# Kernel optimization log

Hardware: AMD Instinct MI355X
Metric: run time of the kernel (lower is better)

## Reference

```python
import jax, jax.numpy as jnp
import numpy as np

NH, HS, K = 32, 2048, 16
HD = HS // NH
B, L = 4, 2048
EPS = 1e-6

def _ln(x, gamma, beta):
    mu = x.mean(-1, keepdims=True)
    var = x.var(-1, keepdims=True)  # ddof=0 == torch unbiased=False
    return gamma * ((x - mu) / jnp.sqrt(var + EPS)) + beta

def _ln_fused_l2_bwd(x, target, gamma, beta):
    D = x.shape[-1]
    mu = x.mean(-1, keepdims=True)
    std = jnp.sqrt(x.var(-1, keepdims=True) + EPS)
    xh = (x - mu) / std
    gxh = (gamma * xh + beta - target) * gamma
    return (D * gxh - gxh.sum(-1, keepdims=True) - xh * (gxh * xh).sum(-1, keepdims=True)) / (D * std)

def setup_inputs() -> dict:
    key = jax.random.key(0)
    ks = jax.random.split(key, 8)
    s = 0.02
    return {
        'hidden_states': jax.random.normal(ks[0], (B, L, HS), jnp.float32),
        'position_ids': jnp.tile(jnp.arange(L, dtype=jnp.int32)[None], (B, 1)),
        'q_w': jax.random.normal(ks[1], (HS, HS), jnp.float32) * s,
        'k_w': jax.random.normal(ks[2], (HS, HS), jnp.float32) * s,
        'v_w': jax.random.normal(ks[3], (HS, HS), jnp.float32) * s,
        'o_w': jax.random.normal(ks[4], (HS, HS), jnp.float32) * s,
        'W1': jax.random.normal(ks[5], (NH, HD, HD), jnp.float32) * s,
        'b1': jnp.zeros((NH, 1, HD), jnp.float32),
        'ttt_norm_weight': jnp.ones((NH, HD), jnp.float32),
        'ttt_norm_bias': jnp.zeros((NH, HD), jnp.float32),
        'ttt_lr_weight': jax.random.normal(ks[6], (NH, 1, HS), jnp.float32) * s,
        'ttt_lr_bias': jnp.zeros((NH, 1), jnp.float32),
        'learnable_token_idx': jnp.zeros((K,), jnp.float32),
        'post_norm_weight': jnp.ones((HS,), jnp.float32),
        'post_norm_bias': jnp.zeros((HS,), jnp.float32),
    }

def _forward(hidden_states, q_w, k_w, v_w, o_w, W1, b1, ttt_norm_weight,
             ttt_norm_bias, ttt_lr_weight, ttt_lr_bias, learnable_token_idx,
             post_norm_weight, post_norm_bias):
    Bb, Ll, _ = hidden_states.shape
    NM = Ll // K

    def proj_heads(w):
        return (hidden_states @ w.T).reshape(Bb, Ll, NH, HD).transpose(0, 2, 1, 3)

    XQ = proj_heads(q_w).reshape(Bb, NH, NM, K, HD)
    XK = proj_heads(k_w).reshape(Bb, NH, NM, K, HD)
    XV = proj_heads(v_w).reshape(Bb, NH, NM, K, HD)
    X = hidden_states.reshape(Bb, NM, K, HS)

    # eta: learned per-token lr gate, [B,nh,NM,K,K]
    ttt_lr = jnp.einsum('bnkc,hdc->bhnkd', X, ttt_lr_weight) + ttt_lr_bias.reshape(1, NH, 1, 1, 1)
    ttt_lr_eta = jax.nn.sigmoid(ttt_lr).transpose(0, 1, 2, 4, 3) / HD  # ttt_base_lr = 1.0
    token_idx = jnp.clip(1.0 / jnp.arange(1, K + 1, dtype=jnp.float32) + learnable_token_idx, 0.0, None)
    eta = token_idx.reshape(1, 1, 1, K, 1) * ttt_lr_eta

    ln_w = ttt_norm_weight.reshape(NH, 1, HD)
    ln_b = ttt_norm_bias.reshape(NH, 1, HD)

    def step(carry, x):
        W1_s, b1_s = carry                 # [B,nh,hd,hd], [B,nh,1,hd]
        xq, xk, xv, eta_mb = x             # [B,nh,K,hd], eta_mb [B,nh,K,K]
        Z1 = xk @ W1_s + b1_s
        grad = _ln_fused_l2_bwd(Z1, xv - xk, ln_w, ln_b)
        Attn1 = jnp.tril(xq @ xk.swapaxes(-1, -2))
        b1_bar = b1_s - jnp.tril(eta_mb) @ grad
        Z1_bar = xq @ W1_s - (eta_mb * Attn1) @ grad + b1_bar
        last_eta = eta_mb[:, :, -1, :, None]  # [B,nh,K,1]
        W1_new = W1_s - (last_eta * xk).swapaxes(-1, -2) @ grad
        b1_new = b1_s - jnp.sum(last_eta * grad, axis=-2, keepdims=True)
        out = xq + _ln(Z1_bar, ln_w, ln_b)
        return (W1_new, b1_new), out

    init = (jnp.tile(W1[None], (Bb, 1, 1, 1)), jnp.tile(b1[None], (Bb, 1, 1, 1)))
    xs = (XQ.transpose(2, 0, 1, 3, 4), XK.transpose(2, 0, 1, 3, 4),
          XV.transpose(2, 0, 1, 3, 4), eta.transpose(2, 0, 1, 3, 4))
    _, ys = jax.lax.scan(step, init, xs)          # [NM,B,nh,K,hd]
    out = ys.transpose(1, 0, 3, 2, 4).reshape(Bb, Ll, HS)
    out = _ln(out, post_norm_weight, post_norm_bias)  # post_norm (eps 1e-6)
    return out @ o_w.T

def reference(hidden_states, position_ids, q_w, k_w, v_w, o_w, W1, b1,
              ttt_norm_weight, ttt_norm_bias, ttt_lr_weight, ttt_lr_bias,
              learnable_token_idx, post_norm_weight, post_norm_bias):
    del position_ids  # unused in the shown forward (rope never applied)
    return _forward(hidden_states, q_w, k_w, v_w, o_w, W1, b1, ttt_norm_weight,
                    ttt_norm_bias, ttt_lr_weight, ttt_lr_bias, learnable_token_idx,
                    post_norm_weight, post_norm_bias)
```

## Files before the change

### kernel.cpp

```cpp
#include <hip/hip_runtime.h>

typedef unsigned short u16;
typedef unsigned int u32;
typedef __bf16 bf16_t;
typedef bf16_t bf16x4 __attribute__((ext_vector_type(4)));
typedef bf16_t bf16x8 __attribute__((ext_vector_type(8)));
typedef float f32x4 __attribute__((ext_vector_type(4)));
typedef u16 u16x4 __attribute__((ext_vector_type(4)));
typedef u16 u16x8 __attribute__((ext_vector_type(8)));
typedef short s16x4 __attribute__((ext_vector_type(4)));

#define B_   4
#define L_   2048
#define HS_  2048
#define NH_  32
#define HD_  64
#define KK_  16
#define NM_  128
#define M_   (B_*L_)

__device__ __forceinline__ u16 f2bf(float f) {
  unsigned u = __float_as_uint(f);
  u += 0x7FFFu + ((u >> 16) & 1u);
  return (u16)(u >> 16);
}
__device__ __forceinline__ float bf2f(u16 u) {
  return __uint_as_float(((unsigned)u) << 16);
}
__device__ __forceinline__ s16x4 pk4(float a, float b, float c, float d) {
  bf16x4 v;
  v[0] = (__bf16)a; v[1] = (__bf16)b; v[2] = (__bf16)c; v[3] = (__bf16)d;
  return __builtin_bit_cast(s16x4, v);
}

__device__ __forceinline__ f32x4 mfma16(s16x4 a, s16x4 b, f32x4 c) {
  return __builtin_amdgcn_mfma_f32_16x16x16bf16_1k(a, b, c, 0, 0, 0);
}

template <int CTRL>
__device__ __forceinline__ float dpp_add(float v) {
  int t = __builtin_amdgcn_update_dpp(0, __builtin_bit_cast(int, v), CTRL, 0xF, 0xF, true);
  return v + __builtin_bit_cast(float, t);
}
template <int CTRL>
__device__ __forceinline__ f32x4 dpp_add4(f32x4 v) {
  f32x4 r;
#pragma unroll
  for (int i = 0; i < 4; ++i) r[i] = dpp_add<CTRL>(v[i]);
  return r;
}
__device__ __forceinline__ f32x4 row_reduce16(f32x4 v) {
  v = dpp_add4<0x121>(v);
  v = dpp_add4<0x122>(v);
  v = dpp_add4<0x124>(v);
  v = dpp_add4<0x128>(v);
  return v;
}

__global__ __launch_bounds__(256) void cast_f32_bf16(const float* __restrict__ in,
                                                     u16* __restrict__ out, int n) {
  int i = (blockIdx.x * 256 + threadIdx.x) * 8;
  if (i >= n) return;
  float4 a = *(const float4*)(in + i);
  float4 b = *(const float4*)(in + i + 4);
  u16x8 o;
  o[0]=f2bf(a.x); o[1]=f2bf(a.y); o[2]=f2bf(a.z); o[3]=f2bf(a.w);
  o[4]=f2bf(b.x); o[5]=f2bf(b.y); o[6]=f2bf(b.z); o[7]=f2bf(b.w);
  *(u16x8*)(out + i) = o;
}

#define BM 128
#define BN 128
#define BK 32
#define LDT 40

template <bool BF16OUT>
__global__ __launch_bounds__(256) void gemm_nt(const u16* __restrict__ A,
                                               const u16* __restrict__ Bt,
                                               void* __restrict__ Cv,
                                               int M, int N, int K) {
  __shared__ u16 As[BM * LDT];
  __shared__ u16 Bs[BN * LDT];
  int tid  = threadIdx.x;
  int lane = tid & 63, wave = tid >> 6;
  int quad = lane >> 4, l16 = lane & 15;
  int bM = blockIdx.x * BM, bN = blockIdx.y * BN;
  int wM = (wave >> 1) * 64, wN = (wave & 1) * 64;
  int r0 = tid >> 2, c0 = (tid & 3) * 8;
  const u16* Ap = A + (size_t)bM * K;
  const u16* Bp = Bt + (size_t)bN * K;
  f32x4 acc[4][4] = {};
  u16x8 pa0 = *(const u16x8*)(Ap + (size_t)r0 * K + c0);
  u16x8 pa1 = *(const u16x8*)(Ap + (size_t)(r0 + 64) * K + c0);
  u16x8 pb0 = *(const u16x8*)(Bp + (size_t)r0 * K + c0);
  u16x8 pb1 = *(const u16x8*)(Bp + (size_t)(r0 + 64) * K + c0);
  int nk = K / BK;
  for (int kt = 0; kt < nk; ++kt) {
    *(u16x8*)&As[r0 * LDT + c0]        = pa0;
    *(u16x8*)&As[(r0 + 64) * LDT + c0] = pa1;
    *(u16x8*)&Bs[r0 * LDT + c0]        = pb0;
    *(u16x8*)&Bs[(r0 + 64) * LDT + c0] = pb1;
    __syncthreads();
    if (kt + 1 < nk) {
      int k0 = (kt + 1) * BK + c0;
      pa0 = *(const u16x8*)(Ap + (size_t)r0 * K + k0);
      pa1 = *(const u16x8*)(Ap + (size_t)(r0 + 64) * K + k0);
      pb0 = *(const u16x8*)(Bp + (size_t)r0 * K + k0);
      pb1 = *(const u16x8*)(Bp + (size_t)(r0 + 64) * K + k0);
    }
    bf16x8 af[4], bfr[4];
#pragma unroll
    for (int i = 0; i < 4; ++i) {
      u16x8 t = *(const u16x8*)&As[(wM + i * 16 + l16) * LDT + quad * 8];
      af[i] = __builtin_bit_cast(bf16x8, t);
    }
#pragma unroll
    for (int j = 0; j < 4; ++j) {
      u16x8 t = *(const u16x8*)&Bs[(wN + j * 16 + l16) * LDT + quad * 8];
      bfr[j] = __builtin_bit_cast(bf16x8, t);
    }
#pragma unroll
    for (int i = 0; i < 4; ++i) {
#pragma unroll
      for (int j = 0; j < 4; ++j)
        acc[i][j] = __builtin_amdgcn_mfma_f32_16x16x32_bf16(af[i], bfr[j], acc[i][j], 0, 0, 0);
    }
    __syncthreads();
  }
#pragma unroll
  for (int i = 0; i < 4; ++i) {
#pragma unroll
    for (int j = 0; j < 4; ++j) {
      int row = bM + wM + i * 16 + quad * 4;
      int col = bN + wN + j * 16 + l16;
      if (BF16OUT) {
        u16* cp = (u16*)Cv + (size_t)row * N + col;
#pragma unroll
        for (int r = 0; r < 4; ++r) cp[(size_t)r * N] = f2bf(acc[i][j][r]);
      } else {
        float* cp = (float*)Cv + (size_t)row * N + col;
#pragma unroll
        for (int r = 0; r < 4; ++r) cp[(size_t)r * N] = acc[i][j][r];
      }
    }
  }
}

__global__ __launch_bounds__(256) void sig_kernel(const u16* __restrict__ hsb,
                                                  const u16* __restrict__ lrwb,
                                                  const float* __restrict__ lrb,
                                                  float* __restrict__ Sig) {
  __shared__ u16 Bs[32 * LDT];
  int tid = threadIdx.x;
  int lane = tid & 63, wave = tid >> 6;
  int quad = lane >> 4, l16 = lane & 15;
  int m0 = blockIdx.x * 64 + wave * 16;
  f32x4 acc0 = {}, acc1 = {};
  for (int kt = 0; kt < HS_ / BK; ++kt) {
    int k0 = kt * BK;
    if (tid < 128) {
      int r = tid >> 2, c8 = (tid & 3) * 8;
      *(u16x8*)&Bs[r * LDT + c8] = *(const u16x8*)(lrwb + (size_t)r * HS_ + k0 + c8);
    }
    __syncthreads();
    u16x8 ta = *(const u16x8*)(hsb + (size_t)(m0 + l16) * HS_ + k0 + quad * 8);
    u16x8 t0 = *(const u16x8*)&Bs[l16 * LDT + quad * 8];
    u16x8 t1 = *(const u16x8*)&Bs[(16 + l16) * LDT + quad * 8];
    bf16x8 af  = __builtin_bit_cast(bf16x8, ta);
    bf16x8 bf0 = __builtin_bit_cast(bf16x8, t0);
    bf16x8 bf1 = __builtin_bit_cast(bf16x8, t1);
    acc0 = __builtin_amdgcn_mfma_f32_16x16x32_bf16(af, bf0, acc0, 0, 0, 0);
    acc1 = __builtin_amdgcn_mfma_f32_16x16x32_bf16(af, bf1, acc1, 0, 0, 0);
    __syncthreads();
  }
#pragma unroll
  for (int j = 0; j < 2; ++j) {
    f32x4 a = j ? acc1 : acc0;
    int h = j * 16 + l16;
    float bias = lrb[h];
#pragma unroll
    for (int r = 0; r < 4; ++r) {
      int m = m0 + quad * 4 + r;
      float v = a[r] + bias;
      float s = (1.f / (1.f + expf(-v))) * (1.f / 64.f);
      Sig[(size_t)m * NH_ + h] = s;
    }
  }
}

__global__ __launch_bounds__(64, 1) void ttt_scan_wave(
    const u16* __restrict__ XQ, const u16* __restrict__ XK, const u16* __restrict__ XV,
    const float* __restrict__ Sig, const float* __restrict__ W1_0, const float* __restrict__ b1_0,
    const float* __restrict__ lnw, const float* __restrict__ lnb, const float* __restrict__ lti,
    float* __restrict__ Y) {
  int lane = threadIdx.x;
  int quad = lane >> 4, l16 = lane & 15;
  int bh = blockIdx.x, b = bh >> 5, h = bh & 31;

  s16x4 idB;
#pragma unroll
  for (int jj = 0; jj < 4; ++jj)
    idB[jj] = (l16 == quad * 4 + jj) ? (short)0x3F80 : (short)0;

  f32x4 m2[4][4];
  {
    const float* wsrc = W1_0 + (size_t)h * 4096;
#pragma unroll
    for (int c = 0; c < 4; ++c)
#pragma unroll
      for (int a = 0; a < 4; ++a)
#pragma unroll
        for (int r = 0; r < 4; ++r)
          m2[c][a][r] = wsrc[(size_t)(c * 16 + quad * 4 + r) * 64 + a * 16 + l16];
  }

  f32x4 b1r, gam, bet;
#pragma unroll
  for (int a = 0; a < 4; ++a) {
    b1r[a] = b1_0[h * 64 + a * 16 + l16];
    gam[a] = lnw[h * 64 + a * 16 + l16];
    bet[a] = lnb[h * 64 + a * 16 + l16];
  }
  float tokL  = fmaxf(1.0f / (float)(l16 + 1) + lti[l16], 0.0f);
  float tok15 = fmaxf(1.0f / 16.0f + lti[15], 0.0f);

  size_t gb = ((size_t)(b * L_ + l16)) * HS_ + h * HD_ + quad * 4;
  const float* sigp = Sig + (size_t)(b * L_ + quad * 4) * NH_ + h;

  u16x4 cxk[4], cxq[4], cxv[4];
  f32x4 csig;
#pragma unroll
  for (int c = 0; c < 4; ++c) {
    cxk[c] = *(const u16x4*)(XK + gb + c * 16);
    cxq[c] = *(const u16x4*)(XQ + gb + c * 16);
    cxv[c] = *(const u16x4*)(XV + gb + c * 16);
  }
#pragma unroll
  for (int r = 0; r < 4; ++r) csig[r] = sigp[(size_t)r * NH_];

  for (int n = 0; n < NM_; ++n) {
    s16x4 fwB[4][4];
#pragma unroll
    for (int c = 0; c < 4; ++c)
#pragma unroll
      for (int a = 0; a < 4; ++a)
        fwB[c][a] = pk4(m2[c][a][0], m2[c][a][1], m2[c][a][2], m2[c][a][3]);

    s16x4 fdiff[4];
#pragma unroll
    for (int c = 0; c < 4; ++c) {
      float dv[4];
#pragma unroll
      for (int j = 0; j < 4; ++j) dv[j] = bf2f(cxv[c][j]) - bf2f(cxk[c][j]);
      fdiff[c] = pk4(dv[0], dv[1], dv[2], dv[3]);
    }

    s16x4 fxk[4], fxq[4];
#pragma unroll
    for (int c = 0; c < 4; ++c) {
      fxk[c] = __builtin_bit_cast(s16x4, cxk[c]);
      fxq[c] = __builtin_bit_cast(s16x4, cxq[c]);
    }
    f32x4 sigc = csig;

    if (n + 1 < NM_) {
      size_t g = gb + (size_t)(n + 1) * KK_ * HS_;
#pragma unroll
      for (int c = 0; c < 4; ++c) {
        cxk[c] = *(const u16x4*)(XK + g + c * 16);
        cxq[c] = *(const u16x4*)(XQ + g + c * 16);
        cxv[c] = *(const u16x4*)(XV + g + c * 16);
      }
#pragma unroll
      for (int r = 0; r < 4; ++r)
        csig[r] = sigp[(size_t)((n + 1) * KK_ + r) * NH_];
    }

    f32x4 z1[4] = {}, zq4[4] = {}, atT = {};
    f32x4 ddC[4], xkC[4];
#pragma unroll
    for (int c = 0; c < 4; ++c) {
      f32x4 zz = {};
      atT    = mfma16(fxk[c], fxq[c], atT);
      xkC[c] = mfma16(fxk[c], idB, zz);
      ddC[c] = mfma16(fdiff[c], idB, zz);
#pragma unroll
      for (int a = 0; a < 4; ++a) {
        z1[a]  = mfma16(fxk[c], fwB[c][a], z1[a]);
        zq4[a] = mfma16(fxq[c], fwB[c][a], zq4[a]);
      }
    }

    s16x4 fX[4];
#pragma unroll
    for (int c = 0; c < 4; ++c)
      fX[c] = pk4(-tok15 * xkC[c][0], -tok15 * xkC[c][1],
                  -tok15 * xkC[c][2], -tok15 * xkC[c][3]);

    float cf[4];
#pragma unroll
    for (int r = 0; r < 4; ++r)
      cf[r] = (quad * 4 + r <= l16) ? -tokL * (1.0f + atT[r]) : 0.0f;
    s16x4 fA = pk4(cf[0], cf[1], cf[2], cf[3]);

#pragma unroll
    for (int a = 0; a < 4; ++a)
#pragma unroll
      for (int r = 0; r < 4; ++r) z1[a][r] += b1r[a];
    f32x4 s1 = z1[0] + z1[1] + z1[2] + z1[3];
    f32x4 s2 = z1[0] * z1[0] + z1[1] * z1[1] + z1[2] * z1[2] + z1[3] * z1[3];
    s1 = row_reduce16(s1);
    s2 = row_reduce16(s2);
    f32x4 mu, rstd;
#pragma unroll
    for (int r = 0; r < 4; ++r) {
      mu[r] = s1[r] * (1.0f / 64.0f);
      float var = s2[r] * (1.0f / 64.0f) - mu[r] * mu[r];
      rstd[r] = 1.0f / sqrtf(var + 1e-6f);
    }

    f32x4 xh[4], gxh[4], t1v = {}, t2v = {};
#pragma unroll
    for (int a = 0; a < 4; ++a) {
#pragma unroll
      for (int r = 0; r < 4; ++r) {
        xh[a][r]  = (z1[a][r] - mu[r]) * rstd[r];
        gxh[a][r] = (gam[a] * xh[a][r] + bet[a] - ddC[a][r]) * gam[a];
      }
      t1v = t1v + gxh[a];
      t2v = t2v + gxh[a] * xh[a];
    }
    t1v = row_reduce16(t1v);
    t2v = row_reduce16(t2v);

    s16x4 fG[4];
    float bs[4];
#pragma unroll
    for (int a = 0; a < 4; ++a) {
      float sg[4];
#pragma unroll
      for (int r = 0; r < 4; ++r) {
        float g = (64.0f * gxh[a][r] - t1v[r] - xh[a][r] * t2v[r]) * (rstd[r] * (1.0f / 64.0f));
        sg[r] = sigc[r] * g;
      }
      fG[a] = pk4(sg[0], sg[1], sg[2], sg[3]);
      bs[a] = sg[0] + sg[1] + sg[2] + sg[3];
    }
#pragma unroll
    for (int a = 0; a < 4; ++a) {
      bs[a] += __shfl_xor(bs[a], 16, 64);
      bs[a] += __shfl_xor(bs[a], 32, 64);
    }

    f32x4 zb[4];
#pragma unroll
    for (int a = 0; a < 4; ++a) {
      zb[a] = mfma16(fA, fG[a], zq4[a]);
#pragma unroll
      for (int r = 0; r < 4; ++r) zb[a][r] += b1r[a];
    }
#pragma unroll
    for (int a = 0; a < 4; ++a) b1r[a] -= tok15 * bs[a];

#pragma unroll
    for (int c = 0; c < 4; ++c)
#pragma unroll
      for (int a = 0; a < 4; ++a)
        m2[c][a] = mfma16(fX[c], fG[a], m2[c][a]);

    f32x4 w1s = zb[0] + zb[1] + zb[2] + zb[3];
    f32x4 w2s = zb[0] * zb[0] + zb[1] * zb[1] + zb[2] * zb[2] + zb[3] * zb[3];
    w1s = row_reduce16(w1s);
    w2s = row_reduce16(w2s);
#pragma unroll
    for (int r = 0; r < 4; ++r) {
      float mu2 = w1s[r] * (1.0f / 64.0f);
      float var2 = w2s[r] * (1.0f / 64.0f) - mu2 * mu2;
      float rstd2 = 1.0f / sqrtf(var2 + 1e-6f);
      float* yp = Y + ((size_t)(b * L_ + n * KK_ + quad * 4 + r)) * HS_ + h * HD_ + l16;
#pragma unroll
      for (int a = 0; a < 4; ++a)
        yp[a * 16] = gam[a] * ((zb[a][r] - mu2) * rstd2) + bet[a];
    }
  }
}

__global__ __launch_bounds__(256) void postnorm(const float* __restrict__ Yin,
                                                const u16* __restrict__ XQr,
                                                const float* __restrict__ w,
                                                const float* __restrict__ bb,
                                                u16* __restrict__ Yn) {
  __shared__ float red[8];
  int row = blockIdx.x, tid = threadIdx.x;
  const float* x = Yin + (size_t)row * HS_ + tid * 8;
  float4 v0 = *(const float4*)(x);
  float4 v1 = *(const float4*)(x + 4);
  u16x8 xqv = *(const u16x8*)(XQr + (size_t)row * HS_ + tid * 8);
  float vals[8] = {v0.x, v0.y, v0.z, v0.w, v1.x, v1.y, v1.z, v1.w};
#pragma unroll
  for (int t = 0; t < 8; ++t) vals[t] += bf2f(xqv[t]);
  float s = 0.f, ss = 0.f;
#pragma unroll
  for (int t = 0; t < 8; ++t) { s += vals[t]; ss += vals[t] * vals[t]; }
#pragma unroll
  for (int m = 32; m > 0; m >>= 1) { s += __shfl_xor(s, m, 64); ss += __shfl_xor(ss, m, 64); }
  int wave = tid >> 6, lane = tid & 63;
  if (lane == 0) { red[wave] = s; red[4 + wave] = ss; }
  __syncthreads();
  float S  = red[0] + red[1] + red[2] + red[3];
  float SS = red[4] + red[5] + red[6] + red[7];
  float mu = S * (1.f / 2048.f);
  float var = SS * (1.f / 2048.f) - mu * mu;
  float rstd = 1.f / sqrtf(var + 1e-6f);
  const float* wp = w + tid * 8;
  const float* bp = bb + tid * 8;
  u16x8 o;
#pragma unroll
  for (int t = 0; t < 8; ++t) o[t] = f2bf(wp[t] * ((vals[t] - mu) * rstd) + bp[t]);
  *(u16x8*)(Yn + (size_t)row * HS_ + tid * 8) = o;
}

extern "C" void kernel_launch(void* const* d_in, const int* in_sizes, int n_in,
                              void* d_out, int out_size, void* d_ws, size_t ws_size,
                              hipStream_t stream) {
  (void)in_sizes; (void)n_in; (void)out_size; (void)ws_size;
  const float* hidden = (const float*)d_in[0];
  const float* q_w = (const float*)d_in[2];
  const float* k_w = (const float*)d_in[3];
  const float* v_w = (const float*)d_in[4];
  const float* o_w = (const float*)d_in[5];
  const float* W1  = (const float*)d_in[6];
  const float* b1i = (const float*)d_in[7];
  const float* lnw = (const float*)d_in[8];
  const float* lnb = (const float*)d_in[9];
  const float* lrw = (const float*)d_in[10];
  const float* lrb = (const float*)d_in[11];
  const float* lti = (const float*)d_in[12];
  const float* pnw = (const float*)d_in[13];
  const float* pnb = (const float*)d_in[14];
  float* out = (float*)d_out;

  char* w = (char*)d_ws;
  u16* hsb  = (u16*)w;  w += (size_t)16777216 * 2;
  u16* wb   = (u16*)w;  w += (size_t)4194304 * 2;
  u16* lrwb = (u16*)w;  w += (size_t)65536 * 2;
  u16* XQb  = (u16*)w;  w += (size_t)16777216 * 2;
  u16* XKb  = (u16*)w;  w += (size_t)16777216 * 2;
  u16* XVb  = (u16*)w;  w += (size_t)16777216 * 2;
  float* Sg = (float*)w; w += (size_t)M_ * NH_ * 4;
  u16* Yn = hsb;

  cast_f32_bf16<<<8192, 256, 0, stream>>>(hidden, hsb, 16777216);
  cast_f32_bf16<<<32, 256, 0, stream>>>(lrw, lrwb, 65536);

  sig_kernel<<<128, 256, 0, stream>>>(hsb, lrwb, lrb, Sg);

  dim3 gg(M_ / BM, HS_ / BN);
  cast_f32_bf16<<<2048, 256, 0, stream>>>(q_w, wb, 4194304);
  gemm_nt<true><<<gg, 256, 0, stream>>>(hsb, wb, XQb, M_, HS_, HS_);
  cast_f32_bf16<<<2048, 256, 0, stream>>>(k_w, wb, 4194304);
  gemm_nt<true><<<gg, 256, 0, stream>>>(hsb, wb, XKb, M_, HS_, HS_);
  cast_f32_bf16<<<2048, 256, 0, stream>>>(v_w, wb, 4194304);
  gemm_nt<true><<<gg, 256, 0, stream>>>(hsb, wb, XVb, M_, HS_, HS_);

  ttt_scan_wave<<<128, 64, 0, stream>>>(XQb, XKb, XVb, Sg, W1, b1i, lnw, lnb, lti, out);

  postnorm<<<8192, 256, 0, stream>>>(out, XQb, pnw, pnb, Yn);

  cast_f32_bf16<<<2048, 256, 0, stream>>>(o_w, wb, 4194304);
  gemm_nt<false><<<gg, 256, 0, stream>>>(Yn, wb, out, M_, HS_, HS_);
}
```

Before: 898.0 us.

## Fuse Q/K/V projection GEMMs into one kernel sharing the A tile

Replaces three separate bf16 GEMM launches for Q, K and V with one gemm_qkv kernel. Each block loads the hidden-state A tile once and multiplies it against three weight tiles, using a 128x64 tile per block with register prefetch of the next K slice. The aim is to cut repeated global reads of the large activation matrix and two kernel launches. In exchange it needs three separate weight buffers in workspace and holds more accumulators per thread (96 floats), which may reduce occupancy.

```diff
diff --git a/kernel.cpp b/kernel.cpp
--- a/kernel.cpp
+++ b/kernel.cpp
@@ -146,6 +146,84 @@
   }
 }
 
+__global__ __launch_bounds__(256) void gemm_qkv(const u16* __restrict__ A,
+                                                const u16* __restrict__ Bq,
+                                                const u16* __restrict__ Bk,
+                                                const u16* __restrict__ Bv,
+                                                u16* __restrict__ Xq,
+                                                u16* __restrict__ Xk,
+                                                u16* __restrict__ Xv) {
+  const int K = HS_, N = HS_;
+  __shared__ u16 As[128 * LDT];
+  __shared__ u16 Bs[3][64 * LDT];
+  int tid  = threadIdx.x;
+  int lane = tid & 63, wave = tid >> 6;
+  int quad = lane >> 4, l16 = lane & 15;
+  int bM = blockIdx.x * 128, bN = blockIdx.y * 64;
+  int wM = wave * 32;
+  int r0a = tid >> 1, c0a = (tid & 1) * 16;
+  int r0b = tid >> 2, c0b = (tid & 3) * 8;
+  const u16* Ap = A + (size_t)(bM + r0a) * K + c0a;
+  const u16* Bp[3] = {Bq + (size_t)(bN + r0b) * K + c0b,
+                      Bk + (size_t)(bN + r0b) * K + c0b,
+                      Bv + (size_t)(bN + r0b) * K + c0b};
+  f32x4 acc[3][2][4] = {};
+  u16x8 pa0 = *(const u16x8*)(Ap);
+  u16x8 pa1 = *(const u16x8*)(Ap + 8);
+  u16x8 pb[3];
+#pragma unroll
+  for (int wgt = 0; wgt < 3; ++wgt) pb[wgt] = *(const u16x8*)(Bp[wgt]);
+  int nk = K / BK;
+  for (int kt = 0; kt < nk; ++kt) {
+    *(u16x8*)&As[r0a * LDT + c0a]     = pa0;
+    *(u16x8*)&As[r0a * LDT + c0a + 8] = pa1;
+#pragma unroll
+    for (int wgt = 0; wgt < 3; ++wgt)
+      *(u16x8*)&Bs[wgt][r0b * LDT + c0b] = pb[wgt];
+    __syncthreads();
+    if (kt + 1 < nk) {
+      int k0 = (kt + 1) * BK;
+      pa0 = *(const u16x8*)(Ap + k0);
+      pa1 = *(const u16x8*)(Ap + k0 + 8);
+#pragma unroll
+      for (int wgt = 0; wgt < 3; ++wgt) pb[wgt] = *(const u16x8*)(Bp[wgt] + k0);
+    }
+    bf16x8 af[2];
+#pragma unroll
+    for (int i = 0; i < 2; ++i) {
+      u16x8 t = *(const u16x8*)&As[(wM + i * 16 + l16) * LDT + quad * 8];
+      af[i] = __builtin_bit_cast(bf16x8, t);
+    }
+#pragma unroll
+    for (int wgt = 0; wgt < 3; ++wgt) {
+#pragma unroll
+      for (int j = 0; j < 4; ++j) {
+        u16x8 t = *(const u16x8*)&Bs[wgt][(j * 16 + l16) * LDT + quad * 8];
+        bf16x8 bfr = __builtin_bit_cast(bf16x8, t);
+#pragma unroll
+        for (int i = 0; i < 2; ++i)
+          acc[wgt][i][j] = __builtin_amdgcn_mfma_f32_16x16x32_bf16(af[i], bfr, acc[wgt][i][j], 0, 0, 0);
+      }
+    }
+    __syncthreads();
+  }
+  u16* outs[3] = {Xq, Xk, Xv};
+#pragma unroll
+  for (int wgt = 0; wgt < 3; ++wgt) {
+#pragma unroll
+    for (int i = 0; i < 2; ++i) {
+#pragma unroll
+      for (int j = 0; j < 4; ++j) {
+        int row = bM + wM + i * 16 + quad * 4;
+        int col = bN + j * 16 + l16;
+        u16* cp = outs[wgt] + (size_t)row * N + col;
+#pragma unroll
+        for (int r = 0; r < 4; ++r) cp[(size_t)r * N] = f2bf(acc[wgt][i][j][r]);
+      }
+    }
+  }
+}
+
 __global__ __launch_bounds__(256) void sig_kernel(const u16* __restrict__ hsb,
                                                   const u16* __restrict__ lrwb,
                                                   const float* __restrict__ lrb,
@@ -442,7 +520,9 @@
 
   char* w = (char*)d_ws;
   u16* hsb  = (u16*)w;  w += (size_t)16777216 * 2;
-  u16* wb   = (u16*)w;  w += (size_t)4194304 * 2;
+  u16* wbq  = (u16*)w;  w += (size_t)4194304 * 2;
+  u16* wbk  = (u16*)w;  w += (size_t)4194304 * 2;
+  u16* wbv  = (u16*)w;  w += (size_t)4194304 * 2;
   u16* lrwb = (u16*)w;  w += (size_t)65536 * 2;
   u16* XQb  = (u16*)w;  w += (size_t)16777216 * 2;
   u16* XKb  = (u16*)w;  w += (size_t)16777216 * 2;
@@ -455,18 +535,17 @@
 
   sig_kernel<<<128, 256, 0, stream>>>(hsb, lrwb, lrb, Sg);
 
+  cast_f32_bf16<<<2048, 256, 0, stream>>>(q_w, wbq, 4194304);
+  cast_f32_bf16<<<2048, 256, 0, stream>>>(k_w, wbk, 4194304);
+  cast_f32_bf16<<<2048, 256, 0, stream>>>(v_w, wbv, 4194304);
+  dim3 gq(M_ / 128, HS_ / 64);
+  gemm_qkv<<<gq, 256, 0, stream>>>(hsb, wbq, wbk, wbv, XQb, XKb, XVb);
+
+  ttt_scan_wave<<<128, 64, 0, stream>>>(XQb, XKb, XVb, Sg, W1, b1i, lnw, lnb, lti, out);
+
+  postnorm<<<8192, 256, 0, stream>>>(out, XQb, pnw, pnb, Yn);
+
   dim3 gg(M_ / BM, HS_ / BN);
-  cast_f32_bf16<<<2048, 256, 0, stream>>>(q_w, wb, 4194304);
-  gemm_nt<true><<<gg, 256, 0, stream>>>(hsb, wb, XQb, M_, HS_, HS_);
-  cast_f32_bf16<<<2048, 256, 0, stream>>>(k_w, wb, 4194304);
-  gemm_nt<true><<<gg, 256, 0, stream>>>(hsb, wb, XKb, M_, HS_, HS_);
-  cast_f32_bf16<<<2048, 256, 0, stream>>>(v_w, wb, 4194304);
-  gemm_nt<true><<<gg, 256, 0, stream>>>(hsb, wb, XVb, M_, HS_, HS_);
-
-  ttt_scan_wave<<<128, 64, 0, stream>>>(XQb, XKb, XVb, Sg, W1, b1i, lnw, lnb, lti, out);
-
-  postnorm<<<8192, 256, 0, stream>>>(out, XQb, pnw, pnb, Yn);
-
-  cast_f32_bf16<<<2048, 256, 0, stream>>>(o_w, wb, 4194304);
-  gemm_nt<false><<<gg, 256, 0, stream>>>(Yn, wb, out, M_, HS_, HS_);
-}
+  cast_f32_bf16<<<2048, 256, 0, stream>>>(o_w, wbv, 4194304);
+  gemm_nt<false><<<gg, 256, 0, stream>>>(Yn, wbv, out, M_, HS_, HS_);
+}
```

Result: no change. 893.0 us (-0.6%).
